# Optimization experiments

Measured on AMD Instinct MI355X. Metric: run time of the kernel, lower is better.

The kernel has to match this reference:

```python
import jax, jax.numpy as jnp
import numpy as np

B, T, C = 4, 2048, 1024
N_HEAD = 16
HEAD_DIM = C // N_HEAD

def setup_inputs() -> dict:
    key = jax.random.key(0)
    k1, k2, k3 = jax.random.split(key, 3)
    x = jax.random.normal(k1, (B, T, C), dtype=jnp.float32)
    # nn.Linear(C, 3C, bias=False): weight [3C, C], y = x @ W.T
    w_qkv = jax.random.normal(k2, (3 * C, C), dtype=jnp.float32) * (1.0 / np.sqrt(C))
    w_proj = jax.random.normal(k3, (C, C), dtype=jnp.float32) * (1.0 / np.sqrt(C))
    return {"x": x, "w_qkv": w_qkv, "w_proj": w_proj}

def reference(x, w_qkv, w_proj):
    Bx, Tx, Cx = x.shape
    qkv = x @ w_qkv.T  # [B,T,3C]
    q, k, v = jnp.split(qkv, 3, axis=-1)
    def heads(t):
        return t.reshape(Bx, Tx, N_HEAD, HEAD_DIM).transpose(0, 2, 1, 3)  # [B,H,T,D]
    q, k, v = heads(q), heads(k), heads(v)
    scale = HEAD_DIM ** -0.5
    att = jnp.einsum('bhtd,bhsd->bhts', q, k) * scale  # [B,H,T,T]
    causal = jnp.tril(jnp.ones((Tx, Tx), dtype=bool))
    att = jnp.where(causal[None, None], att, -jnp.inf)
    att = jax.nn.softmax(att, axis=-1)
    y = jnp.einsum('bhts,bhsd->bhtd', att, v)  # [B,H,T,D]
    y = y.transpose(0, 2, 1, 3).reshape(Bx, Tx, Cx)
    return y @ w_proj.T
```

## Files before the change

kernel.cpp:

```cpp
#include <hip/hip_runtime.h>
#include <hip/hip_bf16.h>

typedef __attribute__((ext_vector_type(8))) short bf16x8;
typedef __attribute__((ext_vector_type(4))) float f32x4;
typedef __attribute__((ext_vector_type(4))) unsigned short ushort4v;
typedef __attribute__((ext_vector_type(2))) unsigned uint2v;

__device__ __forceinline__ unsigned short f2bf(float f) {
  union { float f; unsigned u; } v; v.f = f;
  unsigned r = v.u + 0x7FFFu + ((v.u >> 16) & 1u);
  return (unsigned short)(r >> 16);
}

__device__ __forceinline__ unsigned pack_bf2(float lo, float hi) {
  __hip_bfloat162 h = __float22bfloat162_rn(make_float2(lo, hi));
  union { __hip_bfloat162 h; unsigned u; } cv; cv.h = h; return cv.u;
}

__device__ __forceinline__ void gll16(const void* g, void* l) {
  __builtin_amdgcn_global_load_lds((const __attribute__((address_space(1))) void*)g,
                                   (__attribute__((address_space(3))) void*)l, 16, 0, 0);
}

#define MFMA16(a, b, c) __builtin_amdgcn_mfma_f32_16x16x32_bf16((a), (b), (c), 0, 0, 0)

__global__ void cvt_f32_bf16(const float* __restrict__ s, unsigned short* __restrict__ d, int n) {
  int i = (blockIdx.x * blockDim.x + threadIdx.x) * 4;
  if (i >= n) return;
  float4 f = *(const float4*)(s + i);
  ushort4v r;
  r[0] = f2bf(f.x); r[1] = f2bf(f.y); r[2] = f2bf(f.z); r[3] = f2bf(f.w);
  *(ushort4v*)(d + i) = r;
}

template<int EPI>
__global__ __launch_bounds__(512, 1)
void gemm8(const unsigned short* __restrict__ A,
           const unsigned short* __restrict__ B,
           unsigned short* __restrict__ obf,
           float* __restrict__ of32,
           int M, int N, int K) {
  extern __shared__ unsigned short lds[];
  const int tid = threadIdx.x, wid = tid >> 6, lane = tid & 63;
  const int c = lane & 15, g = lane >> 4;
  const int wr = wid >> 1, wc = wid & 1;
  const int nbn = N >> 7;
  const int nwg = gridDim.x;
  int wg = (blockIdx.x & 7) * (nwg >> 3) + (blockIdx.x >> 3);
  const int m0 = (wg / nbn) * 256, n0 = (wg % nbn) * 128;
  const int NT = K >> 6;
  const size_t rb = (size_t)K * 2;
  const int swz = (c & 7) << 4;

  const int r8 = lane >> 3;
  const char* Ag = (const char*)A + (size_t)m0 * rb + (size_t)r8 * rb + (size_t)(((lane & 7) ^ r8) * 16);
  const char* Bg = (const char*)B + (size_t)n0 * rb + (size_t)r8 * rb + (size_t)(((lane & 7) ^ r8) * 16);

  auto stageA = [&](int t, int par) {
#pragma unroll
    for (int j = 0; j < 4; ++j) {
      int ch = wid * 4 + j;
      gll16(Ag + (size_t)(ch * 8) * rb + t * 128, lds + par * 16384 + ch * 512);
    }
  };
  auto stageB = [&](int t, int bpar) {
#pragma unroll
    for (int j = 0; j < 2; ++j) {
      int ch = wid * 2 + j;
      gll16(Bg + (size_t)(ch * 8) * rb + t * 128, lds + 32768 + bpar * 8192 + ch * 512);
    }
  };

  f32x4 acc[4][4];
#pragma unroll
  for (int i = 0; i < 4; ++i)
#pragma unroll
    for (int j = 0; j < 4; ++j) acc[i][j] = f32x4{0.f, 0.f, 0.f, 0.f};

  stageA(0, 0); stageB(0, 0); stageA(1, 1); stageB(1, 1);
  asm volatile("s_waitcnt vmcnt(6)" ::: "memory");
  __builtin_amdgcn_s_barrier();

  for (int t = 0; t < NT; ++t) {
    const int cur = t & 1;
    const int bcur = t % 3;
    const unsigned short* Ac = lds + cur * 16384;
    const unsigned short* Bc = lds + 32768 + bcur * 8192;
    bf16x8 af[4][2], bf0[2][2];
#pragma unroll
    for (int mi = 0; mi < 4; ++mi) {
      int arow = wr * 64 + mi * 16 + c;
#pragma unroll
      for (int kk = 0; kk < 2; ++kk)
        af[mi][kk] = *(const bf16x8*)((const char*)Ac + arow * 128 + ((kk * 64 + g * 16) ^ swz));
    }
#pragma unroll
    for (int ni = 0; ni < 2; ++ni) {
      int brow = wc * 64 + ni * 16 + c;
#pragma unroll
      for (int kk = 0; kk < 2; ++kk)
        bf0[ni][kk] = *(const bf16x8*)((const char*)Bc + brow * 128 + ((kk * 64 + g * 16) ^ swz));
    }
    __builtin_amdgcn_s_barrier();
    asm volatile("s_waitcnt lgkmcnt(0)" ::: "memory");
    __builtin_amdgcn_sched_barrier(0);
    __builtin_amdgcn_s_setprio(1);
#pragma unroll
    for (int kk = 0; kk < 2; ++kk)
#pragma unroll
      for (int mi = 0; mi < 4; ++mi)
#pragma unroll
        for (int ni = 0; ni < 2; ++ni)
          acc[mi][ni] = MFMA16(af[mi][kk], bf0[ni][kk], acc[mi][ni]);
    __builtin_amdgcn_s_setprio(0);
    __builtin_amdgcn_s_barrier();
    bf16x8 bf1[2][2];
#pragma unroll
    for (int ni = 0; ni < 2; ++ni) {
      int brow = wc * 64 + (ni + 2) * 16 + c;
#pragma unroll
      for (int kk = 0; kk < 2; ++kk)
        bf1[ni][kk] = *(const bf16x8*)((const char*)Bc + brow * 128 + ((kk * 64 + g * 16) ^ swz));
    }
    const bool more = (t + 2 < NT);
    if (more) { stageA(t + 2, cur); stageB(t + 2, (t + 2) % 3); }
    __builtin_amdgcn_s_barrier();
    asm volatile("s_waitcnt lgkmcnt(0)" ::: "memory");
    __builtin_amdgcn_sched_barrier(0);
    __builtin_amdgcn_s_setprio(1);
#pragma unroll
    for (int kk = 0; kk < 2; ++kk)
#pragma unroll
      for (int mi = 0; mi < 4; ++mi)
#pragma unroll
        for (int ni = 0; ni < 2; ++ni)
          acc[mi][ni + 2] = MFMA16(af[mi][kk], bf1[ni][kk], acc[mi][ni + 2]);
    __builtin_amdgcn_s_setprio(0);
    if (more) { asm volatile("s_waitcnt vmcnt(6)" ::: "memory"); }
    else      { asm volatile("s_waitcnt vmcnt(0)" ::: "memory"); }
    __builtin_amdgcn_s_barrier();
  }

#pragma unroll
  for (int mi = 0; mi < 4; ++mi)
#pragma unroll
    for (int ni = 0; ni < 4; ++ni)
#pragma unroll
      for (int r4 = 0; r4 < 4; ++r4) {
        float v = acc[mi][ni][r4];
        int mg = m0 + wr * 64 + mi * 16 + g * 4 + r4;
        int ng = n0 + wc * 64 + ni * 16 + c;
        if (EPI == 0) {
          int which = ng >> 10, rem = ng & 1023;
          int hh = rem >> 6, dd = rem & 63;
          int bb = mg >> 11, tt = mg & 2047;
          size_t idx = (size_t)which * 8388608u + ((size_t)(bb * 16 + hh) * 2048 + tt) * 64 + dd;
          obf[idx] = f2bf(v);
        } else {
          of32[(size_t)mg * N + ng] = v;
        }
      }
}

__global__ __launch_bounds__(256, 6)
void attn_fwd(const unsigned short* __restrict__ qb,
              const unsigned short* __restrict__ kb,
              const unsigned short* __restrict__ vb,
              unsigned short* __restrict__ yb) {
  __shared__ unsigned short Kt[64 * 64];
  __shared__ unsigned short Vt[64 * 64];
  __shared__ unsigned short Pl[4 * 16 * 72];
  const int tid = threadIdx.x, w = tid >> 6, lane = tid & 63;
  const int c = lane & 15, g = lane >> 4;
  const int bh = blockIdx.x & 63;
  const int qt = 31 - (blockIdx.x >> 6);
  const int q0 = qt * 64;
  const int b = bh >> 4, h = bh & 15;
  const size_t hb = (size_t)bh * 131072;
  const float GAM = 0.125f * 1.44269504089f;

  const unsigned short* qp = qb + hb + (size_t)(q0 + w * 16 + c) * 64;
  bf16x8 qf0 = *(const bf16x8*)(qp + g * 8);
  bf16x8 qf1 = *(const bf16x8*)(qp + 32 + g * 8);

  f32x4 yacc[4];
#pragma unroll
  for (int i = 0; i < 4; ++i) yacc[i] = f32x4{0.f, 0.f, 0.f, 0.f};
  float mrun = -1e30f, lsum = 0.f;
  unsigned short* pw = Pl + w * (16 * 72);

  for (int kv = 0; kv <= qt; ++kv) {
    const int kv0 = kv * 64;
    const bool diag = (kv == qt);
    if (kv) __syncthreads();
#pragma unroll
    for (int r = 0; r < 2; ++r) {
      int chunk = w * 2 + r;
      int row = chunk * 8 + (lane >> 3);
      int bo = (lane & 7) * 16;
      int sbo = bo ^ ((row & 7) << 4);
      gll16((const char*)(kb + hb + (size_t)(kv0 + row) * 64) + sbo, Kt + chunk * 512);
    }
    {
      int kv2 = (lane & 31) * 2;
      int dblk = w * 16 + (lane >> 5) * 8;
      const unsigned short* vp = vb + hb + (size_t)(kv0 + kv2) * 64 + dblk;
      bf16x8 r0 = *(const bf16x8*)(vp);
      bf16x8 r1 = *(const bf16x8*)(vp + 64);
#pragma unroll
      for (int i = 0; i < 8; ++i) {
        int d = dblk + i;
        unsigned pk2 = ((unsigned)(unsigned short)r0[i]) | (((unsigned)(unsigned short)r1[i]) << 16);
        *(unsigned*)(Vt + d * 64 + (kv2 ^ ((d & 7) << 3))) = pk2;
      }
    }
    __syncthreads();

    f32x4 sacc[4];
#pragma unroll
    for (int nt = 0; nt < 4; ++nt) sacc[nt] = f32x4{0.f, 0.f, 0.f, 0.f};
#pragma unroll
    for (int kk = 0; kk < 2; ++kk)
#pragma unroll
      for (int nt = 0; nt < 4; ++nt) {
        int row = nt * 16 + c;
        bf16x8 kf = *(const bf16x8*)(Kt + row * 64 + ((kk * 32 + g * 8) ^ ((row & 7) << 3)));
        sacc[nt] = MFMA16(kf, (kk ? qf1 : qf0), sacc[nt]);
      }

    if (diag) {
      int ql = w * 16 + c;
#pragma unroll
      for (int nt = 0; nt < 4; ++nt)
#pragma unroll
        for (int r = 0; r < 4; ++r)
          if (nt * 16 + g * 4 + r > ql) sacc[nt][r] = -1e30f;
    }

    float m0 = -1e30f;
#pragma unroll
    for (int nt = 0; nt < 4; ++nt) {
      float a = fmaxf(fmaxf(sacc[nt][0], sacc[nt][1]), fmaxf(sacc[nt][2], sacc[nt][3]));
      m0 = fmaxf(m0, a);
    }
    m0 = fmaxf(m0, __shfl_xor(m0, 16));
    m0 = fmaxf(m0, __shfl_xor(m0, 32));

    if (__any(m0 > mrun + 32.0f)) {
      float mnew = fmaxf(mrun, m0);
      float corr = __builtin_amdgcn_exp2f(GAM * (mrun - mnew));
      lsum *= corr;
#pragma unroll
      for (int dt = 0; dt < 4; ++dt) yacc[dt] *= corr;
      mrun = mnew;
    }

    float bexp = -GAM * mrun;
    float psum = 0.f;
#pragma unroll
    for (int nt = 0; nt < 4; ++nt) {
      float p0 = __builtin_amdgcn_exp2f(fmaf(sacc[nt][0], GAM, bexp));
      float p1 = __builtin_amdgcn_exp2f(fmaf(sacc[nt][1], GAM, bexp));
      float p2 = __builtin_amdgcn_exp2f(fmaf(sacc[nt][2], GAM, bexp));
      float p3 = __builtin_amdgcn_exp2f(fmaf(sacc[nt][3], GAM, bexp));
      psum += (p0 + p1) + (p2 + p3);
      uint2v pkv;
      pkv[0] = pack_bf2(p0, p1);
      pkv[1] = pack_bf2(p2, p3);
      *(uint2v*)(pw + c * 72 + nt * 16 + g * 4) = pkv;
    }
    lsum += psum;

#pragma unroll
    for (int kk = 0; kk < 2; ++kk) {
      bf16x8 pb = *(const bf16x8*)(pw + c * 72 + kk * 32 + g * 8);
#pragma unroll
      for (int dt = 0; dt < 4; ++dt) {
        int n = dt * 16 + c;
        bf16x8 vf = *(const bf16x8*)(Vt + n * 64 + ((kk * 32 + g * 8) ^ ((n & 7) << 3)));
        yacc[dt] = MFMA16(vf, pb, yacc[dt]);
      }
    }
  }

  lsum += __shfl_xor(lsum, 16);
  lsum += __shfl_xor(lsum, 32);
  float inv = 1.0f / lsum;
  int row = q0 + w * 16 + c;
  unsigned short* yp = yb + ((size_t)(b * 2048 + row)) * 1024 + h * 64;
#pragma unroll
  for (int dt = 0; dt < 4; ++dt) {
    uint2v pkv;
    pkv[0] = pack_bf2(yacc[dt][0] * inv, yacc[dt][1] * inv);
    pkv[1] = pack_bf2(yacc[dt][2] * inv, yacc[dt][3] * inv);
    *(uint2v*)(yp + dt * 16 + g * 4) = pkv;
  }
}

extern "C" void kernel_launch(void* const* d_in, const int* in_sizes, int n_in,
                              void* d_out, int out_size, void* d_ws, size_t ws_size,
                              hipStream_t stream) {
  const float* x     = (const float*)d_in[0];
  const float* wqkv  = (const float*)d_in[1];
  const float* wproj = (const float*)d_in[2];
  float* out = (float*)d_out;

  unsigned short* ws     = (unsigned short*)d_ws;
  unsigned short* xb     = ws;
  unsigned short* wqkvb  = xb + 8388608;
  unsigned short* wprojb = wqkvb + 3145728;
  unsigned short* qkvb   = wprojb + 1048576;
  unsigned short* yb     = qkvb + 3 * 8388608;

  cvt_f32_bf16<<<8192, 256, 0, stream>>>(x, xb, 8388608);
  cvt_f32_bf16<<<3072, 256, 0, stream>>>(wqkv, wqkvb, 3145728);
  cvt_f32_bf16<<<1024, 256, 0, stream>>>(wproj, wprojb, 1048576);

  gemm8<0><<<768, 512, 114688, stream>>>(xb, wqkvb, qkvb, nullptr, 8192, 3072, 1024);
  attn_fwd<<<2048, 256, 0, stream>>>(qkvb, qkvb + 8388608, qkvb + 2 * 8388608, yb);
  gemm8<1><<<256, 512, 114688, stream>>>(yb, wprojb, nullptr, out, 8192, 1024, 1024);
}
```

Before: 178.9 us.

## Restructure GEMM to 256-wide N tiles with K=32 steps and triple buffering

Replaces the GEMM kernel with a templated variant that uses 256-column N tiles, a 2x4 wave layout, K-steps of 32 and a three-stage LDS ring for both A and B. The QKV projection now uses 256x256 tiles (fewer workgroups, more reuse per tile), while the output projection uses 128x256 tiles. The loads for stage t+2 are split, with A issued before the first MFMA half and B before the second. This is meant to raise arithmetic intensity and overlap loads better. The cost is more loop iterations with shorter MFMA bursts per barrier and different occupancy and tail behaviour.

```diff
diff --git a/kernel.cpp b/kernel.cpp
--- a/kernel.cpp
+++ b/kernel.cpp
@@ -33,123 +33,122 @@
   *(ushort4v*)(d + i) = r;
 }
 
-template<int EPI>
+template<int EPI, int MIF>
 __global__ __launch_bounds__(512, 1)
-void gemm8(const unsigned short* __restrict__ A,
-           const unsigned short* __restrict__ B,
-           unsigned short* __restrict__ obf,
-           float* __restrict__ of32,
-           int M, int N, int K) {
+void gemm4p(const unsigned short* __restrict__ A,
+            const unsigned short* __restrict__ B,
+            unsigned short* __restrict__ obf,
+            float* __restrict__ of32,
+            int M, int N, int K) {
   extern __shared__ unsigned short lds[];
+  constexpr int BM = MIF * 32;
+  constexpr int ABUF = BM * 32;
+  constexpr int BBASE = 3 * ABUF;
   const int tid = threadIdx.x, wid = tid >> 6, lane = tid & 63;
   const int c = lane & 15, g = lane >> 4;
-  const int wr = wid >> 1, wc = wid & 1;
-  const int nbn = N >> 7;
+  const int wm = wid >> 2, wn = wid & 3;
+  const int nbn = N >> 8;
   const int nwg = gridDim.x;
   int wg = (blockIdx.x & 7) * (nwg >> 3) + (blockIdx.x >> 3);
-  const int m0 = (wg / nbn) * 256, n0 = (wg % nbn) * 128;
-  const int NT = K >> 6;
+  const int m0 = (wg / nbn) * BM, n0 = (wg % nbn) * 256;
+  const int NT = K >> 5;
   const size_t rb = (size_t)K * 2;
-  const int swz = (c & 7) << 4;
-
-  const int r8 = lane >> 3;
-  const char* Ag = (const char*)A + (size_t)m0 * rb + (size_t)r8 * rb + (size_t)(((lane & 7) ^ r8) * 16);
-  const char* Bg = (const char*)B + (size_t)n0 * rb + (size_t)r8 * rb + (size_t)(((lane & 7) ^ r8) * 16);
-
-  auto stageA = [&](int t, int par) {
-#pragma unroll
-    for (int j = 0; j < 4; ++j) {
-      int ch = wid * 4 + j;
-      gll16(Ag + (size_t)(ch * 8) * rb + t * 128, lds + par * 16384 + ch * 512);
+  const int swz = (c & 3) << 4;
+
+  const int r16 = lane >> 2;
+  const int sl = (lane & 3) ^ (r16 & 3);
+  const char* Ag = (const char*)A + (size_t)(m0 + r16) * rb + sl * 16;
+  const char* Bg = (const char*)B + (size_t)(n0 + r16) * rb + sl * 16;
+
+  auto stageA = [&](int t, int buf) {
+#pragma unroll
+    for (int j = 0; j < MIF / 4; ++j) {
+      int ch = wid * (MIF / 4) + j;
+      gll16(Ag + (size_t)(ch * 16) * rb + t * 64, lds + buf * ABUF + ch * 512);
     }
   };
-  auto stageB = [&](int t, int bpar) {
+  auto stageB = [&](int t, int buf) {
 #pragma unroll
     for (int j = 0; j < 2; ++j) {
       int ch = wid * 2 + j;
-      gll16(Bg + (size_t)(ch * 8) * rb + t * 128, lds + 32768 + bpar * 8192 + ch * 512);
+      gll16(Bg + (size_t)(ch * 16) * rb + t * 64, lds + BBASE + buf * 8192 + ch * 512);
     }
   };
 
-  f32x4 acc[4][4];
-#pragma unroll
-  for (int i = 0; i < 4; ++i)
+  f32x4 acc[MIF][4];
+#pragma unroll
+  for (int i = 0; i < MIF; ++i)
 #pragma unroll
     for (int j = 0; j < 4; ++j) acc[i][j] = f32x4{0.f, 0.f, 0.f, 0.f};
 
   stageA(0, 0); stageB(0, 0); stageA(1, 1); stageB(1, 1);
-  asm volatile("s_waitcnt vmcnt(6)" ::: "memory");
+  if constexpr (MIF == 8) { asm volatile("s_waitcnt vmcnt(4)" ::: "memory"); }
+  else                    { asm volatile("s_waitcnt vmcnt(3)" ::: "memory"); }
   __builtin_amdgcn_s_barrier();
 
   for (int t = 0; t < NT; ++t) {
-    const int cur = t & 1;
-    const int bcur = t % 3;
-    const unsigned short* Ac = lds + cur * 16384;
-    const unsigned short* Bc = lds + 32768 + bcur * 8192;
-    bf16x8 af[4][2], bf0[2][2];
-#pragma unroll
-    for (int mi = 0; mi < 4; ++mi) {
-      int arow = wr * 64 + mi * 16 + c;
-#pragma unroll
-      for (int kk = 0; kk < 2; ++kk)
-        af[mi][kk] = *(const bf16x8*)((const char*)Ac + arow * 128 + ((kk * 64 + g * 16) ^ swz));
-    }
-#pragma unroll
-    for (int ni = 0; ni < 2; ++ni) {
-      int brow = wc * 64 + ni * 16 + c;
-#pragma unroll
-      for (int kk = 0; kk < 2; ++kk)
-        bf0[ni][kk] = *(const bf16x8*)((const char*)Bc + brow * 128 + ((kk * 64 + g * 16) ^ swz));
-    }
+    const int cur = t % 3;
+    const unsigned short* Ac = lds + cur * ABUF;
+    const unsigned short* Bc = lds + BBASE + cur * 8192;
+    const bool more = (t + 2 < NT);
+    const int nbuf = (t + 2) % 3;
+    bf16x8 af[MIF], bfr[4];
+#pragma unroll
+    for (int mi = 0; mi < MIF / 2; ++mi) {
+      int arow = wm * (MIF * 16) + mi * 16 + c;
+      af[mi] = *(const bf16x8*)((const char*)Ac + arow * 64 + ((g * 16) ^ swz));
+    }
+#pragma unroll
+    for (int ni = 0; ni < 4; ++ni) {
+      int brow = wn * 64 + ni * 16 + c;
+      bfr[ni] = *(const bf16x8*)((const char*)Bc + brow * 64 + ((g * 16) ^ swz));
+    }
+    if (more) stageA(t + 2, nbuf);
     __builtin_amdgcn_s_barrier();
     asm volatile("s_waitcnt lgkmcnt(0)" ::: "memory");
     __builtin_amdgcn_sched_barrier(0);
     __builtin_amdgcn_s_setprio(1);
 #pragma unroll
-    for (int kk = 0; kk < 2; ++kk)
-#pragma unroll
-      for (int mi = 0; mi < 4; ++mi)
-#pragma unroll
-        for (int ni = 0; ni < 2; ++ni)
-          acc[mi][ni] = MFMA16(af[mi][kk], bf0[ni][kk], acc[mi][ni]);
+    for (int mi = 0; mi < MIF / 2; ++mi)
+#pragma unroll
+      for (int ni = 0; ni < 4; ++ni)
+        acc[mi][ni] = MFMA16(af[mi], bfr[ni], acc[mi][ni]);
     __builtin_amdgcn_s_setprio(0);
     __builtin_amdgcn_s_barrier();
-    bf16x8 bf1[2][2];
-#pragma unroll
-    for (int ni = 0; ni < 2; ++ni) {
-      int brow = wc * 64 + (ni + 2) * 16 + c;
-#pragma unroll
-      for (int kk = 0; kk < 2; ++kk)
-        bf1[ni][kk] = *(const bf16x8*)((const char*)Bc + brow * 128 + ((kk * 64 + g * 16) ^ swz));
-    }
-    const bool more = (t + 2 < NT);
-    if (more) { stageA(t + 2, cur); stageB(t + 2, (t + 2) % 3); }
+#pragma unroll
+    for (int mi = MIF / 2; mi < MIF; ++mi) {
+      int arow = wm * (MIF * 16) + mi * 16 + c;
+      af[mi] = *(const bf16x8*)((const char*)Ac + arow * 64 + ((g * 16) ^ swz));
+    }
+    if (more) stageB(t + 2, nbuf);
     __builtin_amdgcn_s_barrier();
     asm volatile("s_waitcnt lgkmcnt(0)" ::: "memory");
     __builtin_amdgcn_sched_barrier(0);
     __builtin_amdgcn_s_setprio(1);
 #pragma unroll
-    for (int kk = 0; kk < 2; ++kk)
-#pragma unroll
-      for (int mi = 0; mi < 4; ++mi)
-#pragma unroll
-        for (int ni = 0; ni < 2; ++ni)
-          acc[mi][ni + 2] = MFMA16(af[mi][kk], bf1[ni][kk], acc[mi][ni + 2]);
+    for (int mi = MIF / 2; mi < MIF; ++mi)
+#pragma unroll
+      for (int ni = 0; ni < 4; ++ni)
+        acc[mi][ni] = MFMA16(af[mi], bfr[ni], acc[mi][ni]);
     __builtin_amdgcn_s_setprio(0);
-    if (more) { asm volatile("s_waitcnt vmcnt(6)" ::: "memory"); }
-    else      { asm volatile("s_waitcnt vmcnt(0)" ::: "memory"); }
+    if (more) {
+      if constexpr (MIF == 8) { asm volatile("s_waitcnt vmcnt(4)" ::: "memory"); }
+      else                    { asm volatile("s_waitcnt vmcnt(3)" ::: "memory"); }
+    } else {
+      asm volatile("s_waitcnt vmcnt(0)" ::: "memory");
+    }
     __builtin_amdgcn_s_barrier();
   }
 
 #pragma unroll
-  for (int mi = 0; mi < 4; ++mi)
+  for (int mi = 0; mi < MIF; ++mi)
 #pragma unroll
     for (int ni = 0; ni < 4; ++ni)
 #pragma unroll
       for (int r4 = 0; r4 < 4; ++r4) {
         float v = acc[mi][ni][r4];
-        int mg = m0 + wr * 64 + mi * 16 + g * 4 + r4;
-        int ng = n0 + wc * 64 + ni * 16 + c;
+        int mg = m0 + wm * (MIF * 16) + mi * 16 + g * 4 + r4;
+        int ng = n0 + wn * 64 + ni * 16 + c;
         if (EPI == 0) {
           int which = ng >> 10, rem = ng & 1023;
           int hh = rem >> 6, dd = rem & 63;
@@ -316,7 +315,7 @@
   cvt_f32_bf16<<<3072, 256, 0, stream>>>(wqkv, wqkvb, 3145728);
   cvt_f32_bf16<<<1024, 256, 0, stream>>>(wproj, wprojb, 1048576);
 
-  gemm8<0><<<768, 512, 114688, stream>>>(xb, wqkvb, qkvb, nullptr, 8192, 3072, 1024);
+  gemm4p<0, 8><<<384, 512, 98304, stream>>>(xb, wqkvb, qkvb, nullptr, 8192, 3072, 1024);
   attn_fwd<<<2048, 256, 0, stream>>>(qkvb, qkvb + 8388608, qkvb + 2 * 8388608, yb);
-  gemm8<1><<<256, 512, 114688, stream>>>(yb, wprojb, nullptr, out, 8192, 1024, 1024);
-}
+  gemm4p<1, 4><<<256, 512, 73728, stream>>>(yb, wprojb, nullptr, out, 8192, 1024, 1024);
+}
```

Result: slower. 185.3 us (+3.6%).
